# Performance work log

Hardware: AMD Instinct MI355X
Metric: run time of the kernel (lower is better)

Reference implementation:

```python
import jax, jax.numpy as jnp
import numpy as np

# sarModule stage: in=256, out=512, blocks=2, stride=2, patch_groups=4, mask_size=7
B, C_IN, H, W = 32, 256, 56, 56
C_OUT = 512
PLANES = C_OUT // 4   # Bottleneck inner width = planes // expansion = 128
G = 4                 # patch_groups
MS = 7                # mask_size
TEMP = 1.0            # gumbel-softmax temperature


def conv(x, w, stride=1, pad=0, groups=1):
    return jax.lax.conv_general_dilated(
        x, w, (stride, stride), [(pad, pad), (pad, pad)],
        feature_group_count=groups,
        dimension_numbers=('NCHW', 'OIHW', 'NCHW'))


def bn(x, g, b):
    # BatchNorm in inference form with running_mean=0, running_var=1 folded in
    return x * g[None, :, None, None] + b[None, :, None, None]


def avgpool3s2(x):
    # nn.AvgPool2d(3, stride=2, padding=1), count_include_pad=True
    s = jax.lax.reduce_window(x, 0.0, jax.lax.add, (1, 1, 3, 3), (1, 1, 2, 2),
                              [(0, 0), (0, 0), (1, 1), (1, 1)])
    return s / 9.0


def setup_inputs() -> dict:
    key = jax.random.key(0)
    ks = iter(jax.random.split(key, 64))

    def w(shape):
        fan_in = int(np.prod(shape[1:]))
        return jax.random.normal(next(ks), shape, jnp.float32) * np.float32((2.0 / fan_in) ** 0.5)

    ones = lambda n: jnp.ones((n,), jnp.float32)
    zeros = lambda n: jnp.zeros((n,), jnp.float32)

    x = jax.random.normal(next(ks), (B, C_IN, H, W), jnp.float32)
    u = jax.random.uniform(next(ks), (B, 2, G, MS, MS), jnp.float32, 1e-6, 1.0 - 1e-6)
    gumbel_noise = -jnp.log(-jnp.log(u))

    return dict(
        x=x, gumbel_noise=gumbel_noise,
        # base Bottleneck (256->512, stride 2, downsample = avgpool + 1x1 conv + bn)
        b_w1=w((PLANES, C_IN, 1, 1)), b_g1=ones(PLANES), b_b1=zeros(PLANES),
        b_w2=w((PLANES, PLANES, 3, 3)), b_g2=ones(PLANES), b_b2=zeros(PLANES),
        b_w3=w((C_OUT, PLANES, 1, 1)), b_g3=ones(C_OUT), b_b3=zeros(C_OUT),
        b_dw=w((C_OUT, C_IN, 1, 1)), b_dg=ones(C_OUT), b_db=zeros(C_OUT),
        # refine Bottleneck (256->512, stride 1, downsample = 1x1 conv + bn)
        r_w1=w((PLANES, C_IN, 1, 1)), r_g1=ones(PLANES), r_b1=zeros(PLANES),
        r_w2=w((PLANES, PLANES, 3, 3)), r_g2=ones(PLANES), r_b2=zeros(PLANES),
        r_w3=w((C_OUT, PLANES, 1, 1)), r_g3=ones(C_OUT), r_b3=zeros(C_OUT),
        r_dw=w((C_OUT, C_IN, 1, 1)), r_dg=ones(C_OUT), r_db=zeros(C_OUT),
        # maskGen: grouped 3x3 conv (512 -> 4*G), bn, pool, grouped 1x1 fc (4*G -> 2*G)
        m_w=w((4 * G, C_OUT // G, 3, 3)), m_g=ones(4 * G), m_b=zeros(4 * G),
        m_fcw=w((2 * G, 4, 1, 1)),
        m_fcb=jnp.concatenate([0.1 * ones(G), 5.0 * ones(G)]),  # bias init from maskGen
        # fusion Bottleneck (512->512, stride 2, downsample = avgpool only)
        f_w1=w((PLANES, C_OUT, 1, 1)), f_g1=ones(PLANES), f_b1=zeros(PLANES),
        f_w2=w((PLANES, PLANES, 3, 3)), f_g2=ones(PLANES), f_b2=zeros(PLANES),
        f_w3=w((C_OUT, PLANES, 1, 1)), f_g3=ones(C_OUT), f_b3=zeros(C_OUT),
    )


def reference(x, gumbel_noise,
              b_w1, b_g1, b_b1, b_w2, b_g2, b_b2, b_w3, b_g3, b_b3, b_dw, b_dg, b_db,
              r_w1, r_g1, r_b1, r_w2, r_g2, r_b2, r_w3, r_g3, r_b3, r_dw, r_dg, r_db,
              m_w, m_g, m_b, m_fcw, m_fcb,
              f_w1, f_g1, f_b1, f_w2, f_g2, f_b2, f_w3, f_g3, f_b3):
    # ---- base branch: Bottleneck stride 2, last_relu=False -> [B,512,28,28]
    o = jax.nn.relu(bn(conv(x, b_w1), b_g1, b_b1))
    o = jax.nn.relu(bn(conv(o, b_w2, stride=2, pad=1), b_g2, b_b2))
    o = bn(conv(o, b_w3), b_g3, b_b3)
    x_base = o + bn(conv(avgpool3s2(x), b_dw), b_dg, b_db)

    # ---- maskGen on x_base
    gmap = jax.nn.relu(bn(conv(x_base, m_w, pad=1, groups=G), m_g, m_b))      # [B,16,28,28]
    hb = x_base.shape[2] // MS                                                 # adaptive avgpool 28->7
    gmap = gmap.reshape(B, 4 * G, MS, hb, MS, hb).mean(axis=(3, 5))            # [B,16,7,7]
    logits = conv(gmap, m_fcw, groups=G) + m_fcb[None, :, None, None]          # [B,8,7,7]
    logits = logits.reshape(B, 2, G, MS, MS)                                   # view(B,2,groups,ms,ms)
    # hard gumbel-softmax over dim 1 with straight-through estimator
    y = jax.nn.softmax((logits + gumbel_noise) / TEMP, axis=1)
    hard = jax.nn.one_hot(jnp.argmax(y, axis=1), 2, axis=1, dtype=y.dtype)
    gates = hard + y - jax.lax.stop_gradient(y)
    mask = gates[:, 1]                                                         # [B,G,7,7]

    # nearest-upsample mask x8 and expand across each channel group
    mask_up = jnp.repeat(jnp.repeat(mask, H // MS, axis=-2), W // MS, axis=-1) # [B,G,56,56]
    mask_full = jnp.broadcast_to(mask_up[:, :, None], (B, G, C_OUT // G, H, W)).reshape(B, C_OUT, H, W)

    # ---- refine branch: Bottleneck stride 1, output gated by mask, last_relu=False
    o = jax.nn.relu(bn(conv(x, r_w1), r_g1, r_b1))
    o = jax.nn.relu(bn(conv(o, r_w2, pad=1), r_g2, r_b2))
    o = bn(conv(o, r_w3), r_g3, r_b3) * mask_full
    x_refine = o + bn(conv(x, r_dw), r_dg, r_db)                               # [B,512,56,56]

    # ---- fuse: bilinear upsample base to refine resolution (align_corners=False)
    x_base_up = jax.image.resize(x_base, (B, C_OUT, H, W), 'bilinear')
    fused = jax.nn.relu(x_base_up + x_refine)

    # ---- fusion Bottleneck: stride 2, downsample = avgpool only, last_relu=True
    o = jax.nn.relu(bn(conv(fused, f_w1), f_g1, f_b1))
    o = jax.nn.relu(bn(conv(o, f_w2, stride=2, pad=1), f_g2, f_b2))
    o = bn(conv(o, f_w3), f_g3, f_b3)
    out = jax.nn.relu(o + avgpool3s2(fused))                                   # [B,512,28,28]
    return out, mask
```

## Files before the change

kernel.cpp:

```cpp
#include <hip/hip_runtime.h>
#include <cstdint>

#define BB   32
#define CINX 256
#define HH   56
#define WW   56
#define HWX  3136
#define CO   512
#define PL   128
#define HP   28
#define WP   28
#define HWP  784
#define NG   4
#define MSZ  7

typedef unsigned short ushortT;
typedef unsigned int   uint32;
typedef __attribute__((ext_vector_type(8))) short short8;
typedef __attribute__((ext_vector_type(4))) float f32x4;

__device__ __forceinline__ ushortT f2bf(float f){
  uint32 u = __float_as_uint(f);
  u = (u + 0x7fffu + ((u >> 16) & 1u)) >> 16;
  return (ushortT)u;
}
__device__ __forceinline__ float bf2f(ushortT u){
  return __uint_as_float(((uint32)u) << 16);
}
__device__ __forceinline__ void split2(float v, ushortT& h, ushortT& lo){
  h = f2bf(v);
  lo = f2bf(v - bf2f(h));
}
__device__ __forceinline__ uint32 packu(ushortT a, ushortT b){
  return (uint32)a | ((uint32)b << 16);
}

typedef __attribute__((address_space(1))) const void g_void;
typedef __attribute__((address_space(3))) void l_void;
__device__ __forceinline__ void glds16(const ushortT* g, ushortT* l){
  __builtin_amdgcn_global_load_lds((g_void*)g, (l_void*)l, 16, 0, 0);
}

__device__ __forceinline__ void wsplit(float v, ushortT* dh, ushortT* dl, size_t i){
  ushortT h, lo; split2(v, h, lo); dh[i] = h; dl[i] = lo;
}

__global__ __launch_bounds__(256) void prep_w(
  const float* __restrict__ b_w1, const float* __restrict__ b_g1,
  const float* __restrict__ b_w2, const float* __restrict__ b_g2,
  const float* __restrict__ b_w3, const float* __restrict__ b_g3,
  const float* __restrict__ b_dw, const float* __restrict__ b_dg,
  const float* __restrict__ r_w1, const float* __restrict__ r_g1,
  const float* __restrict__ r_w2, const float* __restrict__ r_g2,
  const float* __restrict__ r_w3, const float* __restrict__ r_g3,
  const float* __restrict__ r_dw, const float* __restrict__ r_dg,
  const float* __restrict__ f_w1, const float* __restrict__ f_g1,
  const float* __restrict__ f_w2, const float* __restrict__ f_g2,
  const float* __restrict__ f_w3, const float* __restrict__ f_g3,
  const float* __restrict__ b_b1, const float* __restrict__ r_b1,
  ushortT* __restrict__ dh, ushortT* __restrict__ dl,
  ushortT* __restrict__ zp, float* __restrict__ biasC)
{
  const int idx = blockIdx.x*256 + threadIdx.x;
  switch (blockIdx.y){
    case 0: {
      if (idx >= 32768) return; int m = idx >> 8;
      wsplit(b_w1[idx]*b_g1[m], dh, dl, (size_t)0 + idx); } break;
    case 3: {
      if (idx >= 32768) return; int m = idx >> 8;
      wsplit(r_w1[idx]*r_g1[m], dh, dl, 32768 + (size_t)idx); } break;
    case 1: {
      if (idx >= 147456) return; int m = idx / 1152; int k = idx - m*1152;
      int tap = k >> 7, c = k & 127;
      wsplit(b_w2[((size_t)(m*128 + c))*9 + tap]*b_g2[m], dh, dl, 65536 + (size_t)idx); } break;
    case 2: {
      if (idx >= 196608) return; int m = idx / 384; int k = idx - m*384;
      float v = (k < 128) ? b_w3[m*128 + k]*b_g3[m] : b_dw[m*256 + (k-128)]*b_dg[m];
      wsplit(v, dh, dl, 212992 + (size_t)idx); } break;
    case 4: {
      if (idx >= 147456) return; int m = idx / 1152; int k = idx - m*1152;
      int tap = k >> 7, c = k & 127;
      wsplit(r_w2[((size_t)(m*128 + c))*9 + tap]*r_g2[m], dh, dl, 409600 + (size_t)idx); } break;
    case 5: {
      if (idx >= 196608) return; int m = idx / 384; int k = idx - m*384;
      float v = (k < 128) ? r_w3[m*128 + k]*r_g3[m] : r_dw[m*256 + (k-128)]*r_dg[m];
      wsplit(v, dh, dl, 557056 + (size_t)idx); } break;
    case 6: {
      if (idx >= 65536) return; int m = idx >> 9;
      wsplit(f_w1[idx]*f_g1[m], dh, dl, 753664 + (size_t)idx); } break;
    case 7: {
      if (idx >= 147456) return; int m = idx / 1152; int k = idx - m*1152;
      int tap = k >> 7, c = k & 127;
      wsplit(f_w2[((size_t)(m*128 + c))*9 + tap]*f_g2[m], dh, dl, 819200 + (size_t)idx); } break;
    case 8: {
      if (idx >= 65536) return; int m = idx >> 7;
      wsplit(f_w3[idx]*f_g3[m], dh, dl, 966656 + (size_t)idx); } break;
    case 9: {
      if (idx < 64) zp[idx] = 0;
      if (idx < 128) biasC[idx] = b_b1[idx];
      else if (idx < 256) biasC[idx] = r_b1[idx-128];
    } break;
  }
}

__global__ __launch_bounds__(256) void k_avgpool_x(const float* __restrict__ x, float* __restrict__ out){
  int idx = blockIdx.x*256 + threadIdx.x;
  if (idx >= BB*CINX*HWP) return;
  int p = idx % HWP; int bc = idx / HWP;
  int ox = p % WP, oy = p / WP;
  const float* src = x + (size_t)bc*HWX;
  float s = 0.f;
  #pragma unroll
  for (int dy=0; dy<3; dy++){
    int yy = 2*oy-1+dy;
    if ((unsigned)yy >= HH) continue;
    #pragma unroll
    for (int dx=0; dx<3; dx++){
      int xx = 2*ox-1+dx;
      if ((unsigned)xx >= WW) continue;
      s += src[yy*WW + xx];
    }
  }
  out[idx] = s * (1.f/9.f);
}

__global__ __launch_bounds__(256) void prep_p(const float* __restrict__ t,
    ushortT* __restrict__ ph_, ushortT* __restrict__ pl_){
  __shared__ float s[16][17];
  const int p0 = blockIdx.x*16, c0 = blockIdx.y*16, bz = blockIdx.z;
  const int ci = threadIdx.x >> 4, pi = threadIdx.x & 15;
  s[ci][pi] = t[((size_t)bz*CINX + c0 + ci)*HWP + p0 + pi];
  __syncthreads();
  const int pr = threadIdx.x >> 4, cj = threadIdx.x & 15;
  float v = s[cj][pr];
  ushortT h, lo; split2(v, h, lo);
  size_t o = ((size_t)bz*HWP + p0 + pr)*CINX + c0 + cj;
  ph_[o] = h; pl_[o] = lo;
}

__global__ __launch_bounds__(256) void k_poolf(const ushortT* __restrict__ fzh,
    const ushortT* __restrict__ fzl, float* __restrict__ pf){
  const int p = blockIdx.x, bz = blockIdx.y;
  const int oy = p / WP, ox = p - oy*WP;
  const int c = threadIdx.x*2;
  float s0 = 0.f, s1 = 0.f;
  #pragma unroll
  for (int dy=0; dy<3; dy++){
    const int iy = 2*oy - 1 + dy;
    if ((unsigned)iy >= (unsigned)HH) continue;
    #pragma unroll
    for (int dx=0; dx<3; dx++){
      const int ix = 2*ox - 1 + dx;
      if ((unsigned)ix >= (unsigned)WW) continue;
      const size_t fi = ((size_t)bz*HWX + (size_t)(iy*WW + ix))*CO + c;
      uint32 hh = *(const uint32*)(fzh + fi);
      uint32 ll = *(const uint32*)(fzl + fi);
      s0 += bf2f((ushortT)(hh & 0xffff)) + bf2f((ushortT)(ll & 0xffff));
      s1 += bf2f((ushortT)(hh >> 16))    + bf2f((ushortT)(ll >> 16));
    }
  }
  const size_t o = ((size_t)bz*HWP + p)*CO + c;
  pf[o]   = s0 * (1.f/9.f);
  pf[o+1] = s1 * (1.f/9.f);
}

template<int KIND,int EPI,int S1F,int S2F,int MT,int STRIDE,int PAD,int HIN,int WIN,
         int WOUT,int NOUT,int C1,int C2,int BSTR1,int MTOT,int KTOT>
__global__ __launch_bounds__(MT*2)
void gemm_bf3(const ushortT* __restrict__ wph, const ushortT* __restrict__ wpl,
              const ushortT* __restrict__ s1h, const ushortT* __restrict__ s1l,
              const ushortT* __restrict__ s2h, const ushortT* __restrict__ s2l,
              const float* __restrict__ xf32,
              const float* __restrict__ bias1, const float* __restrict__ bias2,
              const float* __restrict__ maskf, const float* __restrict__ xbase,
              const ushortT* __restrict__ zp,
              ushortT* __restrict__ oh, ushortT* __restrict__ ol,
              float* __restrict__ of32)
{
  constexpr int NW = MT/32;
  constexpr int BCALLS = 8/NW;
  constexpr bool GATHER1 = (KIND==0 && S1F==1);
  constexpr bool GATHER2 = (KIND>=2 && S2F==1);
  __shared__ ushortT smem[MT*64 + 8192];
  ushortT* AH  = smem;
  ushortT* AL  = smem + MT*32;
  ushortT* BHs = smem + MT*64;
  ushortT* BLs = smem + MT*64 + 4096;

  const int tid = threadIdx.x;
  const int nt = blockIdx.x, mt = blockIdx.y, bz = blockIdx.z;
  const int l  = tid & 63, w = tid >> 6;
  const int wm = w >> 1, wn = w & 1;

  size_t a_src[2]; int a_dst[2];
  #pragma unroll
  for (int c=0;c<2;c++){
    int s = (w*2 + c)*64 + l;
    int row = s >> 2, slotm = s & 3;
    int logical = slotm ^ ((row >> 1) & 3);
    a_src[c] = (size_t)(mt*MT + row)*KTOT + logical*8;
    a_dst[c] = (w*2 + c)*512;
  }

  int b_dst[2]; size_t b_base1[2], b_base2[2]; int b_klane[2];
  int b_oy[2], b_ox[2]; bool b_ok[2]; float b_mv[2];
  #pragma unroll
  for (int c=0;c<BCALLS;c++){
    int s = (w*BCALLS + c)*64 + l;
    int row = s >> 2, slotm = s & 3;
    int logical = slotm ^ ((row >> 1) & 3);
    b_klane[c] = logical*8;
    b_dst[c] = (w*BCALLS + c)*512;
    int ngr = nt*128 + row;
    b_ok[c] = (ngr < NOUT);
    int oyv = ngr / WOUT, oxv = ngr - (ngr / WOUT)*WOUT;
    b_oy[c] = oyv; b_ox[c] = oxv;
    b_base1[c] = ((size_t)bz*NOUT + ngr)*BSTR1 + b_klane[c];
    b_base2[c] = ((size_t)bz*NOUT + ngr)*C2 + b_klane[c];
    b_mv[c] = 1.f;
    if (KIND == 3)
      b_mv[c] = b_ok[c] ? maskf[((size_t)(bz*NG + mt)*MSZ + (oyv>>3))*MSZ + (oxv>>3)] : 0.f;
  }

  const int sr = tid >> 1;
  const int hp = tid & 1;
  const int swz = (sr >> 1) & 3;
  const int lws0 = sr*32 + ((2*hp) ^ swz)*8;
  const int lws1 = sr*32 + ((2*hp + 1) ^ swz)*8;
  const int ng = nt*128 + sr;

  f32x4 acc[4][4];
  f32x4 zf = {0.f,0.f,0.f,0.f};
  #pragma unroll
  for (int i=0;i<4;i++)
    #pragma unroll
    for (int j=0;j<4;j++) acc[i][j] = zf;

  const int NK = KTOT / 32;
  for (int ks=0; ks<NK; ks++){
    const int k0 = ks*32;
    #pragma unroll
    for (int c=0;c<2;c++){
      glds16(wph + a_src[c] + k0, AH + a_dst[c]);
      glds16(wpl + a_src[c] + k0, AL + a_dst[c]);
    }
    if constexpr (GATHER1){
      if (tid < 256){
        uint4 b0 = make_uint4(0,0,0,0), b1v = b0, b2v = b0, b3v = b0;
        if (ng < NOUT){
          size_t fbase = ((size_t)bz*C1 + k0 + hp*16)*(size_t)NOUT + ng;
          ushortT h[16], lo[16];
          #pragma unroll
          for (int e=0;e<16;e++){ split2(xf32[fbase + (size_t)e*NOUT], h[e], lo[e]); }
          b0  = make_uint4(packu(h[0],h[1]),  packu(h[2],h[3]),  packu(h[4],h[5]),  packu(h[6],h[7]));
          b1v = make_uint4(packu(h[8],h[9]),  packu(h[10],h[11]),packu(h[12],h[13]),packu(h[14],h[15]));
          b2v = make_uint4(packu(lo[0],lo[1]),packu(lo[2],lo[3]),packu(lo[4],lo[5]),packu(lo[6],lo[7]));
          b3v = make_uint4(packu(lo[8],lo[9]),packu(lo[10],lo[11]),packu(lo[12],lo[13]),packu(lo[14],lo[15]));
        }
        *(uint4*)(BHs + lws0) = b0;  *(uint4*)(BHs + lws1) = b1v;
        *(uint4*)(BLs + lws0) = b2v; *(uint4*)(BLs + lws1) = b3v;
      }
    } else if (GATHER2 && k0 >= C1){
      if (tid < 256){
        uint4 b0 = make_uint4(0,0,0,0), b1v = b0, b2v = b0, b3v = b0;
        if (ng < NOUT){
          size_t fbase = ((size_t)bz*C2 + (k0 - C1) + hp*16)*(size_t)NOUT + ng;
          ushortT h[16], lo[16];
          #pragma unroll
          for (int e=0;e<16;e++){ split2(xf32[fbase + (size_t)e*NOUT], h[e], lo[e]); }
          b0  = make_uint4(packu(h[0],h[1]),  packu(h[2],h[3]),  packu(h[4],h[5]),  packu(h[6],h[7]));
          b1v = make_uint4(packu(h[8],h[9]),  packu(h[10],h[11]),packu(h[12],h[13]),packu(h[14],h[15]));
          b2v = make_uint4(packu(lo[0],lo[1]),packu(lo[2],lo[3]),packu(lo[4],lo[5]),packu(lo[6],lo[7]));
          b3v = make_uint4(packu(lo[8],lo[9]),packu(lo[10],lo[11]),packu(lo[12],lo[13]),packu(lo[14],lo[15]));
        }
        *(uint4*)(BHs + lws0) = b0;  *(uint4*)(BHs + lws1) = b1v;
        *(uint4*)(BLs + lws0) = b2v; *(uint4*)(BLs + lws1) = b3v;
      }
    } else {
      #pragma unroll
      for (int c=0;c<BCALLS;c++){
        const ushortT *sh, *sl;
        if constexpr (KIND == 0){
          bool ok = b_ok[c];
          size_t off = b_base1[c] + k0;
          sh = ok ? s1h + off : zp;  sl = ok ? s1l + off : zp;
        } else if constexpr (KIND == 1){
          const int tap = k0 >> 7;
          const int cb  = (k0 & 127);
          const int dy = tap/3, dx = tap - 3*(tap/3);
          int iy = b_oy[c]*STRIDE + dy - PAD;
          int ix = b_ox[c]*STRIDE + dx - PAD;
          bool ok = b_ok[c] && (unsigned)iy < (unsigned)HIN && (unsigned)ix < (unsigned)WIN;
          size_t off = ((size_t)bz*(HIN*WIN) + (size_t)(iy*WIN + ix))*BSTR1 + cb + b_klane[c];
          sh = ok ? s1h + off : zp;  sl = ok ? s1l + off : zp;
        } else {
          if (k0 < C1){
            bool ok = b_ok[c] && (KIND != 3 || b_mv[c] != 0.f);
            size_t off = b_base1[c] + k0;
            sh = ok ? s1h + off : zp;  sl = ok ? s1l + off : zp;
          } else {
            bool ok = b_ok[c];
            size_t off = b_base2[c] + (k0 - C1);
            sh = ok ? s2h + off : zp;  sl = ok ? s2l + off : zp;
          }
        }
        glds16(sh, BHs + b_dst[c]);
        glds16(sl, BLs + b_dst[c]);
      }
    }
    __syncthreads();

    short8 bh[4], bl[4];
    #pragma unroll
    for (int nf=0; nf<4; nf++){
      const int rr = wn*64 + nf*16 + (l & 15);
      const int ph = (l >> 4) ^ ((rr >> 1) & 3);
      bh[nf] = *(const short8*)(BHs + rr*32 + ph*8);
      bl[nf] = *(const short8*)(BLs + rr*32 + ph*8);
    }
    #pragma unroll
    for (int mf=0; mf<4; mf++){
      const int rr = wm*64 + mf*16 + (l & 15);
      const int ph = (l >> 4) ^ ((rr >> 1) & 3);
      short8 ah = *(const short8*)(AH + rr*32 + ph*8);
      short8 al = *(const short8*)(AL + rr*32 + ph*8);
      #pragma unroll
      for (int nf=0; nf<4; nf++)
        acc[mf][nf] = __builtin_amdgcn_mfma_f32_16x16x32_bf16(ah, bh[nf], acc[mf][nf], 0,0,0);
      #pragma unroll
      for (int nf=0; nf<4; nf++)
        acc[mf][nf] = __builtin_amdgcn_mfma_f32_16x16x32_bf16(ah, bl[nf], acc[mf][nf], 0,0,0);
      #pragma unroll
      for (int nf=0; nf<4; nf++)
        acc[mf][nf] = __builtin_amdgcn_mfma_f32_16x16x32_bf16(al, bh[nf], acc[mf][nf], 0,0,0);
    }
    __syncthreads();
  }

  const int mb0 = mt*MT + wm*64;
  const int nb0 = nt*128 + wn*64;

  #pragma unroll
  for (int nf=0; nf<4; nf++){
    const int n = nb0 + nf*16 + (l & 15);
    if (n >= NOUT) continue;
    if constexpr (EPI == 0){
      const size_t ob = ((size_t)bz*NOUT + n)*MTOT;
      #pragma unroll
      for (int mf=0; mf<4; mf++){
        const int m0 = mb0 + mf*16 + (l>>4)*4;
        ushort4 hq, lq; ushortT h0, l0; float v;
        v = fmaxf(acc[mf][nf][0] + bias1[m0+0], 0.f); split2(v,h0,l0); hq.x=h0; lq.x=l0;
        v = fmaxf(acc[mf][nf][1] + bias1[m0+1], 0.f); split2(v,h0,l0); hq.y=h0; lq.y=l0;
        v = fmaxf(acc[mf][nf][2] + bias1[m0+2], 0.f); split2(v,h0,l0); hq.z=h0; lq.z=l0;
        v = fmaxf(acc[mf][nf][3] + bias1[m0+3], 0.f); split2(v,h0,l0); hq.w=h0; lq.w=l0;
        *(ushort4*)(oh + ob + m0) = hq;
        *(ushort4*)(ol + ob + m0) = lq;
      }
    } else if constexpr (EPI == 1){
      #pragma unroll
      for (int mf=0; mf<4; mf++){
        const int m0 = mb0 + mf*16 + (l>>4)*4;
        #pragma unroll
        for (int r=0;r<4;r++){
          const int m = m0 + r;
          of32[((size_t)bz*MTOT + m)*NOUT + n] = acc[mf][nf][r] + bias1[m] + bias2[m];
        }
      }
    } else if constexpr (EPI == 2){
      const int y = n / WOUT, x = n - (n / WOUT)*WOUT;
      const int grpw = (mt*MT + wm*64) >> 7;
      const float mvv = maskf[((size_t)(bz*NG + grpw)*MSZ + (y>>3))*MSZ + (x>>3)];
      const int iy = y >> 1, ix = x >> 1;
      int yA,yB,xA,xB; float wyA,wyB,wxA,wxB;
      if (y & 1){ yA=iy; wyA=0.75f; yB=(iy+1<HP)?iy+1:HP-1; wyB=0.25f; }
      else      { yA=(iy>0)?iy-1:0; wyA=0.25f; yB=iy; wyB=0.75f; }
      if (x & 1){ xA=ix; wxA=0.75f; xB=(ix+1<WP)?ix+1:WP-1; wxB=0.25f; }
      else      { xA=(ix>0)?ix-1:0; wxA=0.25f; xB=ix; wxB=0.75f; }
      const size_t ob = ((size_t)bz*NOUT + n)*MTOT;
      #pragma unroll
      for (int mf=0; mf<4; mf++){
        const int m0 = mb0 + mf*16 + (l>>4)*4;
        ushort4 hq, lq;
        #pragma unroll
        for (int r=0;r<4;r++){
          const int m = m0 + r;
          const float* xb = xbase + ((size_t)bz*MTOT + m)*HWP;
          float up = wyA*(wxA*xb[yA*WP+xA] + wxB*xb[yA*WP+xB])
                   + wyB*(wxA*xb[yB*WP+xA] + wxB*xb[yB*WP+xB]);
          float v = fmaxf(acc[mf][nf][r] + up + mvv*bias1[m] + bias2[m], 0.f);
          ushortT h0, l0; split2(v, h0, l0);
          if      (r==0){hq.x=h0;lq.x=l0;}
          else if (r==1){hq.y=h0;lq.y=l0;}
          else if (r==2){hq.z=h0;lq.z=l0;}
          else          {hq.w=h0;lq.w=l0;}
        }
        *(ushort4*)(oh + ob + m0) = hq;
        *(ushort4*)(ol + ob + m0) = lq;
      }
    } else {
      const float* pfrow = xbase + ((size_t)bz*NOUT + n)*MTOT;
      #pragma unroll
      for (int mf=0; mf<4; mf++){
        const int m0 = mb0 + mf*16 + (l>>4)*4;
        const float4 pv = *(const float4*)(pfrow + m0);
        of32[((size_t)bz*MTOT + m0+0)*NOUT + n] = fmaxf(acc[mf][nf][0] + bias1[m0+0] + pv.x, 0.f);
        of32[((size_t)bz*MTOT + m0+1)*NOUT + n] = fmaxf(acc[mf][nf][1] + bias1[m0+1] + pv.y, 0.f);
        of32[((size_t)bz*MTOT + m0+2)*NOUT + n] = fmaxf(acc[mf][nf][2] + bias1[m0+2] + pv.z, 0.f);
        of32[((size_t)bz*MTOT + m0+3)*NOUT + n] = fmaxf(acc[mf][nf][3] + bias1[m0+3] + pv.w, 0.f);
      }
    }
  }
}

#define GM_LDSW 9216
__global__ __launch_bounds__(256) void k_gmap2(const float* __restrict__ xbase,
    const float* __restrict__ mw, const float* __restrict__ mg, const float* __restrict__ mb,
    float* __restrict__ gmap){
  __shared__ float wsh[GM_LDSW];
  __shared__ float red[16][2][4][16];
  const int tile = blockIdx.x, b = blockIdx.y;
  const int tid = threadIdx.x;
  const int pl = tid & 15, cs = tid >> 4;
  const int p = tile*16 + pl;
  const int oy = p / WP, ox = p - oy*WP;
  int toff[9];
  #pragma unroll
  for (int tap=0; tap<9; tap++){
    int dy = tap/3, dx = tap - 3*dy;
    int yy = oy + dy - 1, xx = ox + dx - 1;
    toff[tap] = ((unsigned)yy < (unsigned)HP && (unsigned)xx < (unsigned)WP) ? (yy*WP + xx) : -1;
  }
  float acc[2][4] = {{0.f,0.f,0.f,0.f},{0.f,0.f,0.f,0.f}};
  for (int pass=0; pass<2; pass++){
    __syncthreads();
    for (int i = tid; i < GM_LDSW; i += 256){
      int ocl = i & 3, tap = (i >> 2) % 9, c_rel = i / 36;
      int cg = pass*256 + c_rel;
      int g = cg >> 7;
      int oc = g*4 + ocl;
      wsh[i] = mw[((size_t)(oc*128 + (cg & 127)))*9 + tap] * mg[oc];
    }
    __syncthreads();
    const float* xb = xbase + ((size_t)b*CO + pass*256 + cs*16)*HWP;
    for (int cl=0; cl<16; cl++){
      const float* xc = xb + (size_t)cl*HWP;
      const float* wr = &wsh[(cs*16 + cl)*36];
      #pragma unroll
      for (int tap=0; tap<9; tap++){
        if (toff[tap] < 0) continue;
        float v = xc[toff[tap]];
        f32x4 w4 = *(const f32x4*)(wr + tap*4);
        acc[pass][0] += v*w4[0];
        acc[pass][1] += v*w4[1];
        acc[pass][2] += v*w4[2];
        acc[pass][3] += v*w4[3];
      }
    }
  }
  #pragma unroll
  for (int pp=0; pp<2; pp++)
    #pragma unroll
    for (int o=0; o<4; o++)
      red[cs][pp][o][pl] = acc[pp][o];
  __syncthreads();
  const int oc = tid >> 4;
  const int g = oc >> 2, ocl = oc & 3, pg = g >> 1, cs0 = (g & 1)*8;
  float s = 0.f;
  #pragma unroll
  for (int t=0; t<8; t++) s += red[cs0 + t][pg][ocl][pl];
  s = fmaxf(s + mb[oc], 0.f);
  gmap[((size_t)b*16 + oc)*HWP + p] = s;
}

__global__ __launch_bounds__(256) void k_gpool(const float* __restrict__ gmap, float* __restrict__ gpool){
  int idx = blockIdx.x*256 + threadIdx.x;
  if (idx >= BB*16*49) return;
  int q = idx % 49; int t = idx / 49; int ch = t % 16; int b = t / 16;
  int my = q/7, mx = q%7;
  const float* src = gmap + ((size_t)b*16 + ch)*HWP;
  float s = 0.f;
  #pragma unroll
  for (int yb=0;yb<4;yb++)
    #pragma unroll
    for (int xb=0;xb<4;xb++)
      s += src[(my*4+yb)*WP + (mx*4+xb)];
  gpool[idx] = s * (1.f/16.f);
}

__global__ __launch_bounds__(256) void k_mask(const float* __restrict__ gpool, const float* __restrict__ fcw,
    const float* __restrict__ fcb, const float* __restrict__ gum,
    float* __restrict__ maskf, float* __restrict__ mout){
  int idx = blockIdx.x*256 + threadIdx.x;
  if (idx >= BB*NG*49) return;
  int q = idx % 49; int t = idx / 49; int g = t % NG; int b = t / NG;
  float lgt[2];
  #pragma unroll
  for (int cls=0; cls<2; cls++){
    int c = cls*NG + g;
    int gc = c >> 1;
    float s = fcb[c];
    #pragma unroll
    for (int k=0;k<4;k++)
      s += fcw[c*4+k] * gpool[((size_t)b*16 + gc*4 + k)*49 + q];
    s += gum[(((size_t)b*2 + cls)*NG + g)*49 + q];
    lgt[cls] = s;
  }
  float m = (lgt[1] > lgt[0]) ? 1.f : 0.f;
  maskf[idx] = m;
  mout[idx] = m;
}

extern "C" void kernel_launch(void* const* d_in, const int* in_sizes, int n_in,
                              void* d_out, int out_size, void* d_ws, size_t ws_size,
                              hipStream_t stream){
  const float* x    = (const float*)d_in[0];
  const float* gum  = (const float*)d_in[1];
  const float* b_w1 = (const float*)d_in[2];
  const float* b_g1 = (const float*)d_in[3];
  const float* b_b1 = (const float*)d_in[4];
  const float* b_w2 = (const float*)d_in[5];
  const float* b_g2 = (const float*)d_in[6];
  const float* b_b2 = (const float*)d_in[7];
  const float* b_w3 = (const float*)d_in[8];
  const float* b_g3 = (const float*)d_in[9];
  const float* b_b3 = (const float*)d_in[10];
  const float* b_dw = (const float*)d_in[11];
  const float* b_dg = (const float*)d_in[12];
  const float* b_db = (const float*)d_in[13];
  const float* r_w1 = (const float*)d_in[14];
  const float* r_g1 = (const float*)d_in[15];
  const float* r_b1 = (const float*)d_in[16];
  const float* r_w2 = (const float*)d_in[17];
  const float* r_g2 = (const float*)d_in[18];
  const float* r_b2 = (const float*)d_in[19];
  const float* r_w3 = (const float*)d_in[20];
  const float* r_g3 = (const float*)d_in[21];
  const float* r_b3 = (const float*)d_in[22];
  const float* r_dw = (const float*)d_in[23];
  const float* r_dg = (const float*)d_in[24];
  const float* r_db = (const float*)d_in[25];
  const float* m_w  = (const float*)d_in[26];
  const float* m_g  = (const float*)d_in[27];
  const float* m_b  = (const float*)d_in[28];
  const float* m_fcw= (const float*)d_in[29];
  const float* m_fcb= (const float*)d_in[30];
  const float* f_w1 = (const float*)d_in[31];
  const float* f_g1 = (const float*)d_in[32];
  const float* f_b1 = (const float*)d_in[33];
  const float* f_w2 = (const float*)d_in[34];
  const float* f_g2 = (const float*)d_in[35];
  const float* f_b2 = (const float*)d_in[36];
  const float* f_w3 = (const float*)d_in[37];
  const float* f_g3 = (const float*)d_in[38];
  const float* f_b3 = (const float*)d_in[39];

  char* ws = (char*)d_ws;
  constexpr size_t O_WPH  = 0;
  constexpr size_t O_WPL  = 2064384;
  constexpr size_t O_CH   = 4128768;
  constexpr size_t O_DH   = 55508992;
  constexpr size_t O_DL   = 61931520;
  constexpr size_t O_EH   = 68354048;
  constexpr size_t O_EL   = 94044160;
  constexpr size_t O_PF   = O_EH;
  constexpr size_t O_XB   = 119734272;
  constexpr size_t O_GMAP = 171114496;
  constexpr size_t O_GPOOL= 172720128;
  constexpr size_t O_MASK = 172820480;
  constexpr size_t O_FH   = 172845568;
  constexpr size_t O_PH   = 172845568;
  constexpr size_t O_PL   = 185690624;
  constexpr size_t O_FL   = 275606016;
  constexpr size_t O_ZP   = 378366464;
  constexpr size_t O_BIASC= 378366592;

  ushortT* WPH = (ushortT*)(ws + O_WPH);
  ushortT* WPL = (ushortT*)(ws + O_WPL);
  ushortT* MGH = (ushortT*)(ws + O_CH);
  ushortT* F1H = (ushortT*)(ws + O_CH);
  ushortT* F1L = (ushortT*)(ws + O_CH + 25690112);
  ushortT* DHp = (ushortT*)(ws + O_DH);
  ushortT* DLp = (ushortT*)(ws + O_DL);
  ushortT* EHp = (ushortT*)(ws + O_EH);
  ushortT* ELp = (ushortT*)(ws + O_EL);
  float*   PF  = (float*)(ws + O_PF);
  float*   XB  = (float*)(ws + O_XB);
  float*   PTMP= (float*)(ws + O_XB);
  ushortT* PHp = (ushortT*)(ws + O_PH);
  ushortT* PLp = (ushortT*)(ws + O_PL);
  ushortT* FHp = (ushortT*)(ws + O_FH);
  ushortT* FLp = (ushortT*)(ws + O_FL);
  float*   GMAP = (float*)(ws + O_GMAP);
  float*   GPOOL= (float*)(ws + O_GPOOL);
  float*   MASKF= (float*)(ws + O_MASK);
  ushortT* ZP  = (ushortT*)(ws + O_ZP);
  float*   BIASC = (float*)(ws + O_BIASC);
  (void)ws_size;

  float* outp = (float*)d_out;
  float* mout = outp + (size_t)BB*CO*HWP;
  ushortT* dout_u = (ushortT*)d_out;

  dim3 blk(256), blk2(512);
  const ushortT* nu = nullptr; const float* nf_ = nullptr;
  ushortT* nuo = nullptr; float* nfo = nullptr;

  prep_w<<<dim3(768, 10), blk, 0, stream>>>(b_w1,b_g1,b_w2,b_g2,b_w3,b_g3,b_dw,b_dg,
      r_w1,r_g1,r_w2,r_g2,r_w3,r_g3,r_dw,r_dg,f_w1,f_g1,f_w2,f_g2,f_w3,f_g3,
      b_b1, r_b1, WPH, WPL, ZP, BIASC);
  k_avgpool_x<<<dim3((BB*CINX*HWP+255)/256), blk, 0, stream>>>(x, PTMP);
  prep_p<<<dim3(49, 16, BB), blk, 0, stream>>>(PTMP, PHp, PLp);

  gemm_bf3<0,0,1,0,256, 1,0,56,56,56,3136, 256,0,256, 256,256><<<dim3(25,1,BB), blk2, 0, stream>>>(
      WPH+0, WPL+0, nu, nu, nu, nu, x, BIASC, nf_, nf_, nf_, ZP, MGH, dout_u, nfo);
  gemm_bf3<1,0,0,0,128, 2,1,56,56,28,784, 128,0,256, 128,1152><<<dim3(7,1,BB), blk, 0, stream>>>(
      WPH+65536, WPL+65536, MGH, dout_u, nu, nu, nf_, b_b2, nf_, nf_, nf_, ZP, DHp, DLp, nfo);
  gemm_bf3<2,1,0,0,256, 1,0,28,28,28,784, 128,256,128, 512,384><<<dim3(7,2,BB), blk2, 0, stream>>>(
      WPH+212992, WPL+212992, DHp, DLp, PHp, PLp, nf_, b_b3, b_db, nf_, nf_, ZP, nuo, nuo, XB);

  k_gmap2<<<dim3(49, BB), blk, 0, stream>>>(XB, m_w, m_g, m_b, GMAP);
  k_gpool<<<dim3(98), blk, 0, stream>>>(GMAP, GPOOL);
  k_mask<<<dim3(25), blk, 0, stream>>>(GPOOL, m_fcw, m_fcb, gum, MASKF, mout);

  gemm_bf3<1,0,0,0,128, 1,1,56,56,56,3136, 128,0,256, 128,1152><<<dim3(25,1,BB), blk, 0, stream>>>(
      WPH+409600, WPL+409600, MGH+128, dout_u+128, nu, nu, nf_, r_b2, nf_, nf_, nf_, ZP, EHp, ELp, nfo);
  gemm_bf3<3,2,0,1,128, 1,0,56,56,56,3136, 128,256,128, 512,384><<<dim3(25,4,BB), blk, 0, stream>>>(
      WPH+557056, WPL+557056, EHp, ELp, nu, nu, x, r_b3, r_db, MASKF, XB, ZP, FHp, FLp, nfo);

  k_poolf<<<dim3(HWP, BB), blk, 0, stream>>>(FHp, FLp, PF);

  gemm_bf3<0,0,0,0,128, 1,0,56,56,56,3136, 512,0,512, 128,512><<<dim3(25,1,BB), blk, 0, stream>>>(
      WPH+753664, WPL+753664, FHp, FLp, nu, nu, nf_, f_b1, nf_, nf_, nf_, ZP, F1H, F1L, nfo);
  gemm_bf3<1,0,0,0,128, 2,1,56,56,28,784, 128,0,128, 128,1152><<<dim3(7,1,BB), blk, 0, stream>>>(
      WPH+819200, WPL+819200, F1H, F1L, nu, nu, nf_, f_b2, nf_, nf_, nf_, ZP, DHp, DLp, nfo);
  gemm_bf3<0,3,0,0,256, 1,0,28,28,28,784, 128,0,128, 512,128><<<dim3(7,2,BB), blk2, 0, stream>>>(
      WPH+966656, WPL+966656, DHp, DLp, nu, nu, nf_, f_b3, nf_, nf_, PF, ZP, nuo, nuo, outp);
}
```

Baseline: 1.104 ms.

## Double-buffer LDS in MT=128 GEMMs, pre-split x, and swap grid order

After: 1.074 ms. -2.7%, faster.

```diff
diff --git a/kernel.cpp b/kernel.cpp
--- a/kernel.cpp
+++ b/kernel.cpp
@@ -138,6 +138,20 @@
   ph_[o] = h; pl_[o] = lo;
 }
 
+__global__ __launch_bounds__(256) void prep_x2(const float* __restrict__ x,
+    ushortT* __restrict__ xh, ushortT* __restrict__ xl){
+  __shared__ float s[16][17];
+  const int p0 = blockIdx.x*16, c0 = blockIdx.y*16, bz = blockIdx.z;
+  const int ci = threadIdx.x >> 4, pi = threadIdx.x & 15;
+  s[ci][pi] = x[((size_t)bz*CINX + c0 + ci)*HWX + p0 + pi];
+  __syncthreads();
+  const int pr = threadIdx.x >> 4, cj = threadIdx.x & 15;
+  float v = s[cj][pr];
+  ushortT h, lo; split2(v, h, lo);
+  size_t o = ((size_t)bz*HWX + p0 + pr)*CINX + c0 + cj;
+  xh[o] = h; xl[o] = lo;
+}
+
 __global__ __launch_bounds__(256) void k_poolf(const ushortT* __restrict__ fzh,
     const ushortT* __restrict__ fzl, float* __restrict__ pf){
   const int p = blockIdx.x, bz = blockIdx.y;
@@ -164,8 +178,8 @@
   pf[o+1] = s1 * (1.f/9.f);
 }
 
-template<int KIND,int EPI,int S1F,int S2F,int MT,int STRIDE,int PAD,int HIN,int WIN,
-         int WOUT,int NOUT,int C1,int C2,int BSTR1,int MTOT,int KTOT>
+template<int KIND,int EPI,int S1F,int MT,int DBUF,int SWAP,int STRIDE,int PAD,
+         int HIN,int WIN,int WOUT,int NOUT,int C1,int C2,int BSTR1,int MTOT,int KTOT>
 __global__ __launch_bounds__(MT*2)
 void gemm_bf3(const ushortT* __restrict__ wph, const ushortT* __restrict__ wpl,
               const ushortT* __restrict__ s1h, const ushortT* __restrict__ s1l,
@@ -180,15 +194,13 @@
   constexpr int NW = MT/32;
   constexpr int BCALLS = 8/NW;
   constexpr bool GATHER1 = (KIND==0 && S1F==1);
-  constexpr bool GATHER2 = (KIND>=2 && S2F==1);
-  __shared__ ushortT smem[MT*64 + 8192];
-  ushortT* AH  = smem;
-  ushortT* AL  = smem + MT*32;
-  ushortT* BHs = smem + MT*64;
-  ushortT* BLs = smem + MT*64 + 4096;
+  constexpr int BUFSZ = MT*64 + 8192;
+  __shared__ ushortT smem[BUFSZ*(DBUF+1)];
 
   const int tid = threadIdx.x;
-  const int nt = blockIdx.x, mt = blockIdx.y, bz = blockIdx.z;
+  const int nt = SWAP ? blockIdx.y : blockIdx.x;
+  const int mt = SWAP ? blockIdx.x : blockIdx.y;
+  const int bz = blockIdx.z;
   const int l  = tid & 63, w = tid >> 6;
   const int wm = w >> 1, wn = w & 1;
 
@@ -236,13 +248,12 @@
     #pragma unroll
     for (int j=0;j<4;j++) acc[i][j] = zf;
 
-  const int NK = KTOT / 32;
-  for (int ks=0; ks<NK; ks++){
+  auto stagef = [&](int ks, ushortT* AHb, ushortT* ALb, ushortT* BHb, ushortT* BLb){
     const int k0 = ks*32;
     #pragma unroll
     for (int c=0;c<2;c++){
-      glds16(wph + a_src[c] + k0, AH + a_dst[c]);
-      glds16(wpl + a_src[c] + k0, AL + a_dst[c]);
+      glds16(wph + a_src[c] + k0, AHb + a_dst[c]);
+      glds16(wpl + a_src[c] + k0, ALb + a_dst[c]);
     }
     if constexpr (GATHER1){
       if (tid < 256){
@@ -257,24 +268,8 @@
           b2v = make_uint4(packu(lo[0],lo[1]),packu(lo[2],lo[3]),packu(lo[4],lo[5]),packu(lo[6],lo[7]));
           b3v = make_uint4(packu(lo[8],lo[9]),packu(lo[10],lo[11]),packu(lo[12],lo[13]),packu(lo[14],lo[15]));
         }
-        *(uint4*)(BHs + lws0) = b0;  *(uint4*)(BHs + lws1) = b1v;
-        *(uint4*)(BLs + lws0) = b2v; *(uint4*)(BLs + lws1) = b3v;
-      }
-    } else if (GATHER2 && k0 >= C1){
-      if (tid < 256){
-        uint4 b0 = make_uint4(0,0,0,0), b1v = b0, b2v = b0, b3v = b0;
-        if (ng < NOUT){
-          size_t fbase = ((size_t)bz*C2 + (k0 - C1) + hp*16)*(size_t)NOUT + ng;
-          ushortT h[16], lo[16];
-          #pragma unroll
-          for (int e=0;e<16;e++){ split2(xf32[fbase + (size_t)e*NOUT], h[e], lo[e]); }
-          b0  = make_uint4(packu(h[0],h[1]),  packu(h[2],h[3]),  packu(h[4],h[5]),  packu(h[6],h[7]));
-          b1v = make_uint4(packu(h[8],h[9]),  packu(h[10],h[11]),packu(h[12],h[13]),packu(h[14],h[15]));
-          b2v = make_uint4(packu(lo[0],lo[1]),packu(lo[2],lo[3]),packu(lo[4],lo[5]),packu(lo[6],lo[7]));
-          b3v = make_uint4(packu(lo[8],lo[9]),packu(lo[10],lo[11]),packu(lo[12],lo[13]),packu(lo[14],lo[15]));
-        }
-        *(uint4*)(BHs + lws0) = b0;  *(uint4*)(BHs + lws1) = b1v;
-        *(uint4*)(BLs + lws0) = b2v; *(uint4*)(BLs + lws1) = b3v;
+        *(uint4*)(BHb + lws0) = b0;  *(uint4*)(BHb + lws1) = b1v;
+        *(uint4*)(BLb + lws0) = b2v; *(uint4*)(BLb + lws1) = b3v;
       }
     } else {
       #pragma unroll
@@ -304,26 +299,28 @@
             sh = ok ? s2h + off : zp;  sl = ok ? s2l + off : zp;
           }
         }
-        glds16(sh, BHs + b_dst[c]);
-        glds16(sl, BLs + b_dst[c]);
+        glds16(sh, BHb + b_dst[c]);
+        glds16(sl, BLb + b_dst[c]);
       }
     }
-    __syncthreads();
-
+  };
+
+  auto computef = [&](const ushortT* AHb, const ushortT* ALb,
+                      const ushortT* BHb, const ushortT* BLb){
     short8 bh[4], bl[4];
     #pragma unroll
     for (int nf=0; nf<4; nf++){
       const int rr = wn*64 + nf*16 + (l & 15);
       const int ph = (l >> 4) ^ ((rr >> 1) & 3);
-      bh[nf] = *(const short8*)(BHs + rr*32 + ph*8);
-      bl[nf] = *(const short8*)(BLs + rr*32 + ph*8);
+      bh[nf] = *(const short8*)(BHb + rr*32 + ph*8);
+      bl[nf] = *(const short8*)(BLb + rr*32 + ph*8);
     }
     #pragma unroll
     for (int mf=0; mf<4; mf++){
       const int rr = wm*64 + mf*16 + (l & 15);
       const int ph = (l >> 4) ^ ((rr >> 1) & 3);
-      short8 ah = *(const short8*)(AH + rr*32 + ph*8);
-      short8 al = *(const short8*)(AL + rr*32 + ph*8);
+      short8 ah = *(const short8*)(AHb + rr*32 + ph*8);
+      short8 al = *(const short8*)(ALb + rr*32 + ph*8);
       #pragma unroll
       for (int nf=0; nf<4; nf++)
         acc[mf][nf] = __builtin_amdgcn_mfma_f32_16x16x32_bf16(ah, bh[nf], acc[mf][nf], 0,0,0);
@@ -334,7 +331,31 @@
       for (int nf=0; nf<4; nf++)
         acc[mf][nf] = __builtin_amdgcn_mfma_f32_16x16x32_bf16(al, bh[nf], acc[mf][nf], 0,0,0);
     }
+  };
+
+  const int NK = KTOT / 32;
+  if constexpr (DBUF == 0){
+    ushortT* AH  = smem;
+    ushortT* AL  = smem + MT*32;
+    ushortT* BHs = smem + MT*64;
+    ushortT* BLs = smem + MT*64 + 4096;
+    for (int ks=0; ks<NK; ks++){
+      stagef(ks, AH, AL, BHs, BLs);
+      __syncthreads();
+      computef(AH, AL, BHs, BLs);
+      __syncthreads();
+    }
+  } else {
+    stagef(0, smem, smem + MT*32, smem + MT*64, smem + MT*64 + 4096);
     __syncthreads();
+    for (int ks=0; ks<NK; ks++){
+      ushortT* cb = smem + (ks & 1)*BUFSZ;
+      ushortT* nb = smem + ((ks & 1) ^ 1)*BUFSZ;
+      if (ks + 1 < NK)
+        stagef(ks + 1, nb, nb + MT*32, nb + MT*64, nb + MT*64 + 4096);
+      computef(cb, cb + MT*32, cb + MT*64, cb + MT*64 + 4096);
+      __syncthreads();
+    }
   }
 
   const int mb0 = mt*MT + wm*64;
@@ -578,6 +599,7 @@
   ushortT* WPH = (ushortT*)(ws + O_WPH);
   ushortT* WPL = (ushortT*)(ws + O_WPL);
   ushortT* MGH = (ushortT*)(ws + O_CH);
+  ushortT* XH  = (ushortT*)(ws + O_CH);
   ushortT* F1H = (ushortT*)(ws + O_CH);
   ushortT* F1L = (ushortT*)(ws + O_CH + 25690112);
   ushortT* DHp = (ushortT*)(ws + O_DH);
@@ -612,28 +634,31 @@
   k_avgpool_x<<<dim3((BB*CINX*HWP+255)/256), blk, 0, stream>>>(x, PTMP);
   prep_p<<<dim3(49, 16, BB), blk, 0, stream>>>(PTMP, PHp, PLp);
 
-  gemm_bf3<0,0,1,0,256, 1,0,56,56,56,3136, 256,0,256, 256,256><<<dim3(25,1,BB), blk2, 0, stream>>>(
+  gemm_bf3<0,0,1,256,0,0, 1,0,56,56,56,3136, 256,0,256, 256,256><<<dim3(25,1,BB), blk2, 0, stream>>>(
       WPH+0, WPL+0, nu, nu, nu, nu, x, BIASC, nf_, nf_, nf_, ZP, MGH, dout_u, nfo);
-  gemm_bf3<1,0,0,0,128, 2,1,56,56,28,784, 128,0,256, 128,1152><<<dim3(7,1,BB), blk, 0, stream>>>(
+  gemm_bf3<1,0,0,128,1,0, 2,1,56,56,28,784, 128,0,256, 128,1152><<<dim3(7,1,BB), blk, 0, stream>>>(
       WPH+65536, WPL+65536, MGH, dout_u, nu, nu, nf_, b_b2, nf_, nf_, nf_, ZP, DHp, DLp, nfo);
-  gemm_bf3<2,1,0,0,256, 1,0,28,28,28,784, 128,256,128, 512,384><<<dim3(7,2,BB), blk2, 0, stream>>>(
+  gemm_bf3<2,1,0,256,0,0, 1,0,28,28,28,784, 128,256,128, 512,384><<<dim3(7,2,BB), blk2, 0, stream>>>(
       WPH+212992, WPL+212992, DHp, DLp, PHp, PLp, nf_, b_b3, b_db, nf_, nf_, ZP, nuo, nuo, XB);
 
   k_gmap2<<<dim3(49, BB), blk, 0, stream>>>(XB, m_w, m_g, m_b, GMAP);
   k_gpool<<<dim3(98), blk, 0, stream>>>(GMAP, GPOOL);
   k_mask<<<dim3(25), blk, 0, stream>>>(GPOOL, m_fcw, m_fcb, gum, MASKF, mout);
 
-  gemm_bf3<1,0,0,0,128, 1,1,56,56,56,3136, 128,0,256, 128,1152><<<dim3(25,1,BB), blk, 0, stream>>>(
+  gemm_bf3<1,0,0,128,1,0, 1,1,56,56,56,3136, 128,0,256, 128,1152><<<dim3(25,1,BB), blk, 0, stream>>>(
       WPH+409600, WPL+409600, MGH+128, dout_u+128, nu, nu, nf_, r_b2, nf_, nf_, nf_, ZP, EHp, ELp, nfo);
-  gemm_bf3<3,2,0,1,128, 1,0,56,56,56,3136, 128,256,128, 512,384><<<dim3(25,4,BB), blk, 0, stream>>>(
-      WPH+557056, WPL+557056, EHp, ELp, nu, nu, x, r_b3, r_db, MASKF, XB, ZP, FHp, FLp, nfo);
+
+  prep_x2<<<dim3(196, 16, BB), blk, 0, stream>>>(x, XH, dout_u);
+
+  gemm_bf3<3,2,0,128,1,1, 1,0,56,56,56,3136, 128,256,128, 512,384><<<dim3(4,25,BB), blk, 0, stream>>>(
+      WPH+557056, WPL+557056, EHp, ELp, XH, dout_u, nf_, r_b3, r_db, MASKF, XB, ZP, FHp, FLp, nfo);
 
   k_poolf<<<dim3(HWP, BB), blk, 0, stream>>>(FHp, FLp, PF);
 
-  gemm_bf3<0,0,0,0,128, 1,0,56,56,56,3136, 512,0,512, 128,512><<<dim3(25,1,BB), blk, 0, stream>>>(
+  gemm_bf3<0,0,0,128,1,0, 1,0,56,56,56,3136, 512,0,512, 128,512><<<dim3(25,1,BB), blk, 0, stream>>>(
       WPH+753664, WPL+753664, FHp, FLp, nu, nu, nf_, f_b1, nf_, nf_, nf_, ZP, F1H, F1L, nfo);
-  gemm_bf3<1,0,0,0,128, 2,1,56,56,28,784, 128,0,128, 128,1152><<<dim3(7,1,BB), blk, 0, stream>>>(
+  gemm_bf3<1,0,0,128,1,0, 2,1,56,56,28,784, 128,0,128, 128,1152><<<dim3(7,1,BB), blk, 0, stream>>>(
       WPH+819200, WPL+819200, F1H, F1L, nu, nu, nf_, f_b2, nf_, nf_, nf_, ZP, DHp, DLp, nfo);
-  gemm_bf3<0,3,0,0,256, 1,0,28,28,28,784, 128,0,128, 512,128><<<dim3(7,2,BB), blk2, 0, stream>>>(
+  gemm_bf3<0,3,0,256,0,0, 1,0,28,28,28,784, 128,0,128, 512,128><<<dim3(7,2,BB), blk2, 0, stream>>>(
       WPH+966656, WPL+966656, DHp, DLp, nu, nu, nf_, f_b3, nf_, nf_, PF, ZP, nuo, nuo, outp);
 }
```
